# Performance work log

Hardware: AMD Instinct MI355X
Metric: run time of the kernel (lower is better)

The kernel has to match this reference:

```python
import jax, jax.numpy as jnp
import numpy as np
from jax import lax

V, D, H, HD, L, E, HID, TOPK, B, T = 32000, 1024, 16, 64, 2, 4, 2048, 2, 1, 1024
EPS = 1e-8


def setup_inputs() -> dict:
    key = jax.random.key(0)
    ks = jax.random.split(key, 10)
    s = 0.02
    so = 0.02 / np.sqrt(2 * L)  # o_proj / down_proj init std
    return dict(
        idx=jax.random.randint(ks[0], (B, T), 0, V),
        tok_emb=jax.random.normal(ks[1], (V, D), jnp.float32) * s,
        attn_norm_w=jnp.ones((L, D), jnp.float32),
        q_w=jax.random.normal(ks[2], (L, D, D), jnp.float32) * s,
        q_b=jnp.zeros((L, D), jnp.float32),
        kv_w=jax.random.normal(ks[3], (L, D, 2 * D), jnp.float32) * s,
        kv_b=jnp.zeros((L, 2 * D), jnp.float32),
        o_w=jax.random.normal(ks[4], (L, D, D), jnp.float32) * so,
        o_b=jnp.zeros((L, D), jnp.float32),
        ffn_norm_w=jnp.ones((L, D), jnp.float32),
        router_w=jax.random.normal(ks[5], (L, D, E), jnp.float32) * s,
        gate_w=jax.random.normal(ks[6], (L, E, D, HID), jnp.float32) * s,
        up_w=jax.random.normal(ks[7], (L, E, D, HID), jnp.float32) * s,
        down_w=jax.random.normal(ks[8], (L, E, HID, D), jnp.float32) * so,
        lnf_w=jnp.ones((D,), jnp.float32),
    )


def _rms(x, w):
    return x / jnp.sqrt(jnp.mean(x * x, axis=-1, keepdims=True) + EPS) * w


def reference(idx, tok_emb, attn_norm_w, q_w, q_b, kv_w, kv_b, o_w, o_b,
              ffn_norm_w, router_w, gate_w, up_w, down_w, lnf_w):
    x = tok_emb[idx]  # [B,T,D]

    # ALiBi bias and causal mask (built once; block_size == T here)
    slopes = jnp.arange(1, H + 1, dtype=jnp.float32) / H          # [H]
    pos = jnp.arange(T, dtype=jnp.float32)
    alibi = slopes[:, None, None] * (pos[None, None, :] - pos[None, :, None])  # [H,T,T]
    causal = jnp.arange(T)[None, :] > jnp.arange(T)[:, None]      # True above diagonal

    for l in range(L):
        # --- causal self-attention with ALiBi ---
        h = _rms(x, attn_norm_w[l])
        q = (h @ q_w[l] + q_b[l]).reshape(B, T, H, HD)
        kv = (h @ kv_w[l] + kv_b[l]).reshape(B, T, 2, H, HD)
        k, v = kv[:, :, 0], kv[:, :, 1]
        att = jnp.einsum('bqhd,bkhd->bhqk', q, k) * (1.0 / np.sqrt(HD))
        att = att + alibi[None]
        att = jnp.where(causal, -jnp.inf, att)
        a = jax.nn.softmax(att, axis=-1)
        y = jnp.einsum('bhqk,bkhd->bqhd', a, v).reshape(B, T, D)
        x = x + y @ o_w[l] + o_b[l]

        # --- MoE FFN (top-k routing, SwiGLU experts, depth-scaled down_proj) ---
        hm = _rms(x, ffn_norm_w[l]).reshape(B * T, D)             # [N,D]
        rlog = hm @ router_w[l]                                   # [N,E]
        vals, sel = lax.top_k(rlog, TOPK)                         # [N,K]
        w = jax.nn.softmax(vals.astype(jnp.float32), axis=-1).astype(hm.dtype)
        # dense per-expert compute, combined sparsely via routing weights
        g = jax.nn.silu(jnp.einsum('nd,edh->enh', hm, gate_w[l])) \
            * jnp.einsum('nd,edh->enh', hm, up_w[l])              # [E,N,HID]
        out_e = jnp.einsum('enh,ehd->end', g, down_w[l]) * (1.0 / np.sqrt(l + 1))
        combine = jnp.sum(jax.nn.one_hot(sel, E, dtype=hm.dtype) * w[..., None], axis=1)  # [N,E]
        moe = jnp.einsum('ne,end->nd', combine, out_e).reshape(B, T, D)
        x = x + moe

    logits = _rms(x, lnf_w) @ tok_emb.T  # tied head weight
    return logits
```

## Files before the change

### kernel.cpp

```cpp
#include <hip/hip_runtime.h>
#include <cmath>

typedef __attribute__((ext_vector_type(8))) _Float16 f16x8;
typedef __attribute__((ext_vector_type(8))) unsigned short u16x8;
typedef __attribute__((ext_vector_type(4))) float f32x4;

#define DEV static __device__ __forceinline__

constexpr int Dm   = 1024;
constexpr int HIDm = 2048;
constexpr int NT   = 1024;
constexpr int NV   = 32000;
constexpr float EPSf  = 1e-8f;
constexpr float LOSC  = 4096.0f;
constexpr float ILOSC = 1.0f / 4096.0f;

DEV unsigned short h2u(_Float16 h){ union{_Float16 h; unsigned short u;} v; v.h=h; return v.u; }

DEV f32x4 MF(f16x8 a, f16x8 b, f32x4 c){ return __builtin_amdgcn_mfma_f32_16x16x32_f16(a,b,c,0,0,0); }

typedef __attribute__((address_space(1))) void GV;
typedef __attribute__((address_space(3))) void LV;
DEV void gll16(const void* g, void* l){
  __builtin_amdgcn_global_load_lds((GV*)(__UINTPTR_TYPE__)g, (LV*)l, 16, 0, 0);
}

template<int SPLIT>
DEV void st_sp(unsigned short* __restrict__ hi, unsigned short* __restrict__ lo, size_t o, float v){
  _Float16 hh = (_Float16)v;
  hi[o] = h2u(hh);
  if constexpr (SPLIT==3) lo[o] = h2u((_Float16)((v - (float)hh)*LOSC));
}

__global__ __launch_bounds__(256) void k_gather(
    const int* __restrict__ idx, const float* __restrict__ emb, float* __restrict__ x)
{
  const int t = blockIdx.x;
  const int d = threadIdx.x*4;
  *(float4*)&x[(size_t)t*Dm + d] = *(const float4*)&emb[(size_t)idx[t]*Dm + d];
}

template<int SPLIT>
__global__ __launch_bounds__(256) void k_rms(
    const float* __restrict__ x, const float* __restrict__ w,
    unsigned short* __restrict__ ohi, unsigned short* __restrict__ olo)
{
  const int t = blockIdx.x, tid = threadIdx.x;
  const float* row = x + (size_t)t*Dm;
  float s = 0.f;
  #pragma unroll
  for (int i=0;i<4;++i){ const float v = row[tid + i*256]; s += v*v; }
  #pragma unroll
  for (int d=1; d<64; d<<=1) s += __shfl_xor(s, d);
  __shared__ float red[4];
  if ((tid&63)==0) red[tid>>6] = s;
  __syncthreads();
  const float tot = red[0]+red[1]+red[2]+red[3];
  const float rstd = rsqrtf(tot*(1.0f/Dm) + EPSf);
  #pragma unroll
  for (int i=0;i<4;++i){
    const int c = tid + i*256;
    st_sp<SPLIT>(ohi, olo, (size_t)t*Dm + c, row[c]*rstd*w[c]);
  }
}

__global__ __launch_bounds__(64) void k_router(
    const float* __restrict__ x, const float* __restrict__ nw,
    const float* __restrict__ rw, float* __restrict__ cmb)
{
  const int t = blockIdx.x, lane = threadIdx.x;
  const float* row = x + (size_t)t*Dm;
  float ss = 0.f;
  for (int i=lane; i<Dm; i+=64) ss += row[i]*row[i];
  #pragma unroll
  for (int d=1; d<64; d<<=1) ss += __shfl_xor(ss, d);
  const float rstd = rsqrtf(ss*(1.0f/Dm) + EPSf);
  float lg0=0,lg1=0,lg2=0,lg3=0;
  for (int i=lane; i<Dm; i+=64){
    const float hm = row[i]*rstd*nw[i];
    lg0 += hm*rw[i*4+0]; lg1 += hm*rw[i*4+1];
    lg2 += hm*rw[i*4+2]; lg3 += hm*rw[i*4+3];
  }
  #pragma unroll
  for (int d=1; d<64; d<<=1){
    lg0 += __shfl_xor(lg0,d); lg1 += __shfl_xor(lg1,d);
    lg2 += __shfl_xor(lg2,d); lg3 += __shfl_xor(lg3,d);
  }
  if (lane==0){
    float lg[4] = {lg0,lg1,lg2,lg3};
    int s0 = 0;
    for (int e=1;e<4;++e) if (lg[e] > lg[s0]) s0 = e;
    int s1 = -1;
    for (int e=0;e<4;++e){ if (e==s0) continue; if (s1<0 || lg[e] > lg[s1]) s1 = e; }
    const float eb2 = expf(lg[s1] - lg[s0]);
    const float inv = 1.0f/(1.0f + eb2);
    float o[4] = {0.f,0.f,0.f,0.f};
    o[s0] = inv; o[s1] = eb2*inv;
    cmb[t*4+0]=o[0]; cmb[t*4+1]=o[1]; cmb[t*4+2]=o[2]; cmb[t*4+3]=o[3];
  }
}

__global__ __launch_bounds__(256) void k_scan(
    const float* __restrict__ cmb, int* __restrict__ tl,
    float* __restrict__ cwl, int* __restrict__ cnt)
{
  const int e = threadIdx.x>>6, lane = threadIdx.x&63;
  int base = 0;
  for (int t0=0; t0<NT; t0+=64){
    const float w = cmb[(size_t)(t0+lane)*4 + e];
    const unsigned long long m = __ballot(w > 0.f);
    const int pre = __popcll(m & ((1ull<<lane)-1ull));
    if (w > 0.f){ tl[e*NT + base + pre] = t0+lane; cwl[e*NT + base + pre] = w; }
    base += __popcll(m);
  }
  if (lane==0) cnt[e] = base;
}

template<int SPLIT>
__global__ __launch_bounds__(256) void k_wconv(
    const float* __restrict__ W, unsigned short* __restrict__ Whi,
    unsigned short* __restrict__ Wlo, int K, int N)
{
  __shared__ float tile[64][65];
  const int t = threadIdx.x;
  const int n0 = blockIdx.x*64, k0 = blockIdx.y*64;
  const size_t eb = (size_t)blockIdx.z * (size_t)K * N;
  const int r = t>>2;
  #pragma unroll
  for (int i=0;i<4;++i){
    const int c = (t&3)*16 + i*4;
    *(float4*)&tile[r][c] = *(const float4*)&W[eb + (size_t)(k0+r)*N + n0 + c];
  }
  __syncthreads();
  const int n = t>>2;
  #pragma unroll
  for (int i=0;i<2;++i){
    const int kc = (t&3)*8 + i*32;
    u16x8 hi, lo;
    #pragma unroll
    for (int j=0;j<8;++j){
      const float v = tile[kc+j][n];
      const _Float16 hh = (_Float16)v;
      hi[j] = h2u(hh);
      if constexpr (SPLIT==3) lo[j] = h2u((_Float16)((v-(float)hh)*LOSC));
      else lo[j] = 0;
    }
    *(u16x8*)&Whi[eb + (size_t)(n0+n)*K + k0 + kc] = hi;
    if constexpr (SPLIT==3) *(u16x8*)&Wlo[eb + (size_t)(n0+n)*K + k0 + kc] = lo;
  }
}

template<int SPLIT, int EPI, int ZMODE>
__global__ __launch_bounds__(256) void k_mm(
    const unsigned short* __restrict__ Ahi, const unsigned short* __restrict__ Alo,
    const unsigned short* __restrict__ Bhi, const unsigned short* __restrict__ Blo,
    const float* __restrict__ bias, const float* __restrict__ bias2,
    unsigned short* __restrict__ Ohi, unsigned short* __restrict__ Olo,
    unsigned short* __restrict__ O2hi, unsigned short* __restrict__ O2lo,
    unsigned short* __restrict__ O3hi, unsigned short* __restrict__ O3lo,
    float* __restrict__ part, int lda, int ldb, int K)
{
  constexpr int PL = (SPLIT==3)?2:1;
  __shared__ __align__(16) unsigned short As[PL][128][32];
  __shared__ __align__(16) unsigned short Bs[PL][128][32];
  const int tid=threadIdx.x, wv=tid>>6, lane=tid&63, fr=lane&15, fg=lane>>4;
  const int n0=blockIdx.x*128, r0=blockIdx.y*128, zz=blockIdx.z;
  const int wr=(wv>>1)*64, wc=(wv&1)*64;
  const int sr=lane>>2, sk=(lane&3)*8;

  const f32x4 z4={0.f,0.f,0.f,0.f};
  f32x4 accM[4][4], accC[4][4];
  #pragma unroll
  for (int i=0;i<4;++i)
    #pragma unroll
    for (int j=0;j<4;++j){ accM[i][j]=z4; accC[i][j]=z4; }

  for (int kt=0; kt<K; kt+=32){
    #pragma unroll
    for (int i=0;i<2;++i){
      const int rr = wv*32 + i*16 + sr;
      size_t ao, bo;
      if constexpr (ZMODE==2){
        ao = (size_t)(r0+rr)*lda + zz*K + kt + sk;
        bo = (size_t)(n0+rr)*ldb + zz*K + kt + sk;
      } else {
        ao = (size_t)(r0+rr)*lda + kt + sk;
        bo = (size_t)(n0+rr)*ldb + kt + sk;
      }
      gll16(&Ahi[ao], &As[0][wv*32+i*16][0]);
      if constexpr (SPLIT==3) gll16(&Alo[ao], &As[1][wv*32+i*16][0]);
      gll16(&Bhi[bo], &Bs[0][wv*32+i*16][0]);
      if constexpr (SPLIT==3) gll16(&Blo[bo], &Bs[1][wv*32+i*16][0]);
    }
    __syncthreads();
    f16x8 a[4][PL], b[4][PL];
    #pragma unroll
    for (int rt=0;rt<4;++rt)
      #pragma unroll
      for (int p=0;p<PL;++p) a[rt][p] = *(const f16x8*)&As[p][wr+rt*16+fr][fg*8];
    #pragma unroll
    for (int ct=0;ct<4;++ct)
      #pragma unroll
      for (int p=0;p<PL;++p) b[ct][p] = *(const f16x8*)&Bs[p][wc+ct*16+fr][fg*8];
    #pragma unroll
    for (int rt=0;rt<4;++rt)
      #pragma unroll
      for (int ct=0;ct<4;++ct){
        accM[rt][ct] = MF(a[rt][0], b[ct][0], accM[rt][ct]);
        if constexpr (SPLIT==3){
          accC[rt][ct] = MF(a[rt][0], b[ct][1], accC[rt][ct]);
          accC[rt][ct] = MF(a[rt][1], b[ct][0], accC[rt][ct]);
        }
      }
    __syncthreads();
  }

  #pragma unroll
  for (int rt=0;rt<4;++rt)
    #pragma unroll
    for (int ct=0;ct<4;++ct)
      #pragma unroll
      for (int j=0;j<4;++j){
        const int row = r0 + wr + rt*16 + fg*4 + j;
        const int col = n0 + wc + ct*16 + fr;
        float v = accM[rt][ct][j];
        if constexpr (SPLIT==3) v += accC[rt][ct][j]*ILOSC;
        if constexpr (EPI==3){
          if (col < Dm){
            v += bias[col];
            st_sp<SPLIT>(Ohi, Olo, (size_t)row*Dm + col, v);
          } else if (col < 2*Dm){
            v += bias2[col-Dm];
            st_sp<SPLIT>(O2hi, O2lo, (size_t)row*Dm + (col-Dm), v);
          } else {
            v += bias2[col-Dm];
            st_sp<SPLIT>(O3hi, O3lo, (size_t)(col-2*Dm)*NT + row, v);
          }
        } else {
          part[((size_t)zz*NT + row)*Dm + col] = v;
        }
      }
}

template<int SPLIT>
__global__ __launch_bounds__(256) void k_down(
    const unsigned short* __restrict__ Ahi, const unsigned short* __restrict__ Alo,
    const unsigned short* __restrict__ Bhi, const unsigned short* __restrict__ Blo,
    const int* __restrict__ tl, const int* __restrict__ cnt,
    float* __restrict__ part)
{
  constexpr int PL = (SPLIT==3)?2:1;
  const int e = blockIdx.z, r0 = blockIdx.y*128, n0 = blockIdx.x*128;
  const int cn = cnt[e];
  if (r0 >= cn) return;
  __shared__ __align__(16) unsigned short As[PL][128][32];
  __shared__ __align__(16) unsigned short Bs[PL][128][32];
  __shared__ int tl_s[128];
  const int tid=threadIdx.x, wv=tid>>6, lane=tid&63, fr=lane&15, fg=lane>>4;
  const int wr=(wv>>1)*64, wc=(wv&1)*64;
  const int sr=lane>>2, sk=(lane&3)*8;
  if (tid < 128) tl_s[tid] = (r0+tid < cn) ? tl[e*NT + r0 + tid] : -1;

  const f32x4 z4={0.f,0.f,0.f,0.f};
  f32x4 accM[4][4], accC[4][4];
  #pragma unroll
  for (int i=0;i<4;++i)
    #pragma unroll
    for (int j=0;j<4;++j){ accM[i][j]=z4; accC[i][j]=z4; }

  for (int kt=0; kt<HIDm; kt+=32){
    #pragma unroll
    for (int i=0;i<2;++i){
      const int rr = wv*32 + i*16 + sr;
      const size_t ao = (size_t)((e<<10) + r0 + rr)*HIDm + kt + sk;
      const size_t bo = (size_t)e*((size_t)Dm*HIDm) + (size_t)(n0+rr)*HIDm + kt + sk;
      gll16(&Ahi[ao], &As[0][wv*32+i*16][0]);
      if constexpr (SPLIT==3) gll16(&Alo[ao], &As[1][wv*32+i*16][0]);
      gll16(&Bhi[bo], &Bs[0][wv*32+i*16][0]);
      if constexpr (SPLIT==3) gll16(&Blo[bo], &Bs[1][wv*32+i*16][0]);
    }
    __syncthreads();
    f16x8 a[4][PL], b[4][PL];
    #pragma unroll
    for (int rt=0;rt<4;++rt)
      #pragma unroll
      for (int p=0;p<PL;++p) a[rt][p] = *(const f16x8*)&As[p][wr+rt*16+fr][fg*8];
    #pragma unroll
    for (int ct=0;ct<4;++ct)
      #pragma unroll
      for (int p=0;p<PL;++p) b[ct][p] = *(const f16x8*)&Bs[p][wc+ct*16+fr][fg*8];
    #pragma unroll
    for (int rt=0;rt<4;++rt)
      #pragma unroll
      for (int ct=0;ct<4;++ct){
        accM[rt][ct] = MF(a[rt][0], b[ct][0], accM[rt][ct]);
        if constexpr (SPLIT==3){
          accC[rt][ct] = MF(a[rt][0], b[ct][1], accC[rt][ct]);
          accC[rt][ct] = MF(a[rt][1], b[ct][0], accC[rt][ct]);
        }
      }
    __syncthreads();
  }

  #pragma unroll
  for (int rt=0;rt<4;++rt)
    #pragma unroll
    for (int ct=0;ct<4;++ct)
      #pragma unroll
      for (int j=0;j<4;++j){
        const int i = wr + rt*16 + fg*4 + j;
        const int col = n0 + wc + ct*16 + fr;
        float v = accM[rt][ct][j];
        if constexpr (SPLIT==3) v += accC[rt][ct][j]*ILOSC;
        const int tok = tl_s[i];
        if (tok >= 0) part[((size_t)e*NT + tok)*Dm + col] = v;
      }
}

template<int SK, bool BIAS>
__global__ __launch_bounds__(256) void k_comb(
    const float* __restrict__ part, const float* __restrict__ bias, float* __restrict__ x)
{
  const int row = blockIdx.x;
  const int c = threadIdx.x*4;
  float4 s = *(float4*)&x[(size_t)row*Dm + c];
  #pragma unroll
  for (int z=0; z<SK; ++z){
    const float4 p = *(const float4*)&part[((size_t)z*NT + row)*Dm + c];
    s.x+=p.x; s.y+=p.y; s.z+=p.z; s.w+=p.w;
  }
  if constexpr (BIAS){
    const float4 b = *(const float4*)&bias[c];
    s.x+=b.x; s.y+=b.y; s.z+=b.z; s.w+=b.w;
  }
  *(float4*)&x[(size_t)row*Dm + c] = s;
}

__global__ __launch_bounds__(256) void k_comb_moe(
    const float* __restrict__ part, const float* __restrict__ cmb, float* __restrict__ x)
{
  const int row = blockIdx.x;
  const int c = threadIdx.x*4;
  float4 s = *(float4*)&x[(size_t)row*Dm + c];
  #pragma unroll
  for (int e=0; e<4; ++e){
    if (cmb[(size_t)row*4 + e] > 0.f){
      const float4 p = *(const float4*)&part[((size_t)e*NT + row)*Dm + c];
      s.x+=p.x; s.y+=p.y; s.z+=p.z; s.w+=p.w;
    }
  }
  *(float4*)&x[(size_t)row*Dm + c] = s;
}

template<int SPLIT>
__global__ __launch_bounds__(512) void k_guf(
    const unsigned short* __restrict__ Ahi, const unsigned short* __restrict__ Alo,
    const unsigned short* __restrict__ Ghi, const unsigned short* __restrict__ Glo,
    const unsigned short* __restrict__ Uhi, const unsigned short* __restrict__ Ulo,
    const int* __restrict__ tl, const float* __restrict__ cwl, const int* __restrict__ cnt,
    unsigned short* __restrict__ Hhi, unsigned short* __restrict__ Hlo, float scale)
{
  constexpr int PL=(SPLIT==3)?2:1;
  const int e = blockIdx.z, r0 = blockIdx.y*128, n0 = blockIdx.x*64;
  const int cn = cnt[e];
  if (r0 >= cn) return;
  __shared__ __align__(16) unsigned short As[PL][128][32];
  __shared__ __align__(16) unsigned short Gs[PL][64][32];
  __shared__ __align__(16) unsigned short Us[PL][64][32];
  __shared__ float cw_s[128];
  const int tid=threadIdx.x, wv=tid>>6, lane=tid&63, fr=lane&15, fg=lane>>4;
  const int wr=(wv>>1)*32, wc=(wv&1)*32;
  const int sr=lane>>2, sk=(lane&3)*8;
  const size_t ebW = (size_t)e * ((size_t)HIDm*Dm);
  if (tid < 128) cw_s[tid] = (r0+tid < cn) ? cwl[e*NT + r0 + tid]*scale : 0.f;

  const int lrA = r0 + wv*16 + sr;
  const int tokA = tl[e*NT + (lrA < cn ? lrA : cn-1)];
  const size_t abase = (size_t)tokA*Dm + sk;
  const int rrB = (wv&3)*16 + sr;
  const size_t bbase = ebW + (size_t)(n0+rrB)*Dm + sk;

  const f32x4 z4={0.f,0.f,0.f,0.f};
  f32x4 aGM[2][2],aGC[2][2],aUM[2][2],aUC[2][2];
  #pragma unroll
  for (int i=0;i<2;++i)
    #pragma unroll
    for (int j=0;j<2;++j){ aGM[i][j]=z4; aGC[i][j]=z4; aUM[i][j]=z4; aUC[i][j]=z4; }

  for (int kt=0; kt<Dm; kt+=32){
    gll16(&Ahi[abase + kt], &As[0][wv*16][0]);
    if constexpr (SPLIT==3) gll16(&Alo[abase + kt], &As[1][wv*16][0]);
    if (wv < 4){
      gll16(&Ghi[bbase + kt], &Gs[0][(wv&3)*16][0]);
      if constexpr (SPLIT==3) gll16(&Glo[bbase + kt], &Gs[1][(wv&3)*16][0]);
    } else {
      gll16(&Uhi[bbase + kt], &Us[0][(wv&3)*16][0]);
      if constexpr (SPLIT==3) gll16(&Ulo[bbase + kt], &Us[1][(wv&3)*16][0]);
    }
    __syncthreads();
    f16x8 a[2][PL], bg[2][PL], bu[2][PL];
    #pragma unroll
    for (int rt=0;rt<2;++rt)
      #pragma unroll
      for (int p=0;p<PL;++p) a[rt][p] = *(const f16x8*)&As[p][wr+rt*16+fr][fg*8];
    #pragma unroll
    for (int ct=0;ct<2;++ct)
      #pragma unroll
      for (int p=0;p<PL;++p){
        bg[ct][p] = *(const f16x8*)&Gs[p][wc+ct*16+fr][fg*8];
        bu[ct][p] = *(const f16x8*)&Us[p][wc+ct*16+fr][fg*8];
      }
    #pragma unroll
    for (int rt=0;rt<2;++rt)
      #pragma unroll
      for (int ct=0;ct<2;++ct){
        aGM[rt][ct] = MF(a[rt][0], bg[ct][0], aGM[rt][ct]);
        aUM[rt][ct] = MF(a[rt][0], bu[ct][0], aUM[rt][ct]);
        if constexpr (SPLIT==3){
          aGC[rt][ct] = MF(a[rt][0], bg[ct][1], aGC[rt][ct]);
          aGC[rt][ct] = MF(a[rt][1], bg[ct][0], aGC[rt][ct]);
          aUC[rt][ct] = MF(a[rt][0], bu[ct][1], aUC[rt][ct]);
          aUC[rt][ct] = MF(a[rt][1], bu[ct][0], aUC[rt][ct]);
        }
      }
    __syncthreads();
  }
  #pragma unroll
  for (int rt=0;rt<2;++rt)
    #pragma unroll
    for (int ct=0;ct<2;++ct)
      #pragma unroll
      for (int j=0;j<4;++j){
        const int i = wr + rt*16 + fg*4 + j;
        const int row = r0 + i;
        const int col = n0 + wc + ct*16 + fr;
        float g = aGM[rt][ct][j], u = aUM[rt][ct][j];
        if constexpr (SPLIT==3){ g += aGC[rt][ct][j]*ILOSC; u += aUC[rt][ct][j]*ILOSC; }
        const float cw = cw_s[i];
        const float h = (g/(1.0f + expf(-g))) * u * cw;
        st_sp<SPLIT>(Hhi, Hlo, (size_t)((e<<10) + row)*HIDm + col, h);
      }
}

__global__ __launch_bounds__(512) void k_lg(
    const unsigned short* __restrict__ Ahi, const float* __restrict__ emb,
    float* __restrict__ out)
{
  __shared__ __align__(16) unsigned short As[256][32];
  __shared__ __align__(16) unsigned short Bs[256][32];
  const int tid=threadIdx.x, wv=tid>>6, lane=tid&63, fr=lane&15, fg=lane>>4;
  const int bid = blockIdx.x;
  const int n0 = (bid>>2)*256, r0 = (bid&3)*256;
  const int wrow=(wv>>2)*128, wcol=(wv&3)*64;
  const int sr=lane>>2, sk=(lane&3)*8;
  const f32x4 z4={0.f,0.f,0.f,0.f};
  f32x4 acc[8][4];
  #pragma unroll
  for (int i=0;i<8;++i)
    #pragma unroll
    for (int j=0;j<4;++j) acc[i][j]=z4;

  for (int kt=0; kt<Dm; kt+=32){
    #pragma unroll
    for (int i=0;i<2;++i){
      const int rr = wv*32 + i*16 + sr;
      gll16(&Ahi[(size_t)(r0+rr)*Dm + kt + sk], &As[wv*32+i*16][0]);
    }
    #pragma unroll
    for (int i=0;i<2;++i){
      const int br = i*128 + (tid>>2);
      const int bc = (tid&3)*8;
      const float* s = &emb[(size_t)(n0+br)*Dm + kt + bc];
      const float4 v0 = *(const float4*)s;
      const float4 v1 = *(const float4*)(s+4);
      u16x8 hh;
      hh[0]=h2u((_Float16)v0.x); hh[1]=h2u((_Float16)v0.y);
      hh[2]=h2u((_Float16)v0.z); hh[3]=h2u((_Float16)v0.w);
      hh[4]=h2u((_Float16)v1.x); hh[5]=h2u((_Float16)v1.y);
      hh[6]=h2u((_Float16)v1.z); hh[7]=h2u((_Float16)v1.w);
      *(u16x8*)&Bs[br][bc] = hh;
    }
    __syncthreads();
    f16x8 a[8], b[4];
    #pragma unroll
    for (int rt=0;rt<8;++rt) a[rt] = *(const f16x8*)&As[wrow+rt*16+fr][fg*8];
    #pragma unroll
    for (int ct=0;ct<4;++ct) b[ct] = *(const f16x8*)&Bs[wcol+ct*16+fr][fg*8];
    #pragma unroll
    for (int rt=0;rt<8;++rt)
      #pragma unroll
      for (int ct=0;ct<4;++ct) acc[rt][ct] = MF(a[rt], b[ct], acc[rt][ct]);
    __syncthreads();
  }
  #pragma unroll
  for (int rt=0;rt<8;++rt)
    #pragma unroll
    for (int ct=0;ct<4;++ct)
      #pragma unroll
      for (int j=0;j<4;++j)
        out[(size_t)(r0+wrow+rt*16+fg*4+j)*NV + n0+wcol+ct*16+fr] = acc[rt][ct][j];
}

template<int SPLIT>
__global__ __launch_bounds__(256) void k_attn(
    const unsigned short* __restrict__ qhi, const unsigned short* __restrict__ qlo,
    const unsigned short* __restrict__ khi, const unsigned short* __restrict__ klo,
    const unsigned short* __restrict__ vthi, const unsigned short* __restrict__ vtlo,
    unsigned short* __restrict__ yhi, unsigned short* __restrict__ ylo)
{
  constexpr int PL = (SPLIT==3) ? 2 : 1;
  const int qt = blockIdx.x, hd = blockIdx.y;
  const int tid = threadIdx.x, wv = tid>>6, lane = tid&63;
  const int fr = lane&15, fg = lane>>4;
  const int rbase = qt*64 + wv*16;
  const float slope = (float)(hd+1) * (1.0f/16.0f);

  __shared__ __align__(16) unsigned short Ps[4][PL][16][32];

  f16x8 aq[2][PL];
  #pragma unroll
  for (int c=0;c<2;++c){
    const size_t off = (size_t)(rbase+fr)*Dm + hd*64 + c*32 + fg*8;
    aq[c][0] = *(const f16x8*)&qhi[off];
    if constexpr (SPLIT==3) aq[c][1] = *(const f16x8*)&qlo[off];
  }

  const f32x4 z4 = {0.f,0.f,0.f,0.f};
  f32x4 yM[4], yC[4];
  #pragma unroll
  for (int ct=0;ct<4;++ct){ yM[ct]=z4; yC[ct]=z4; }
  float m[4], lsum[4];
  #pragma unroll
  for (int j=0;j<4;++j){ m[j] = -INFINITY; lsum[j] = 0.f; }

  const int nkt = qt*2 + 2;
  for (int kt=0; kt<nkt; ++kt){
    f32x4 sM[2], sC[2];
    sM[0]=z4; sM[1]=z4; sC[0]=z4; sC[1]=z4;
    #pragma unroll
    for (int kh=0; kh<2; ++kh){
      #pragma unroll
      for (int c=0;c<2;++c){
        const size_t off = (size_t)(kt*32 + kh*16 + fr)*Dm + hd*64 + c*32 + fg*8;
        const f16x8 b0 = *(const f16x8*)&khi[off];
        sM[kh] = MF(aq[c][0], b0, sM[kh]);
        if constexpr (SPLIT==3){
          const f16x8 b1 = *(const f16x8*)&klo[off];
          sC[kh] = MF(aq[c][0], b1, sC[kh]);
          sC[kh] = MF(aq[c][1], b0, sC[kh]);
        }
      }
    }
    float sv[2][4], mx[4];
    #pragma unroll
    for (int j=0;j<4;++j) mx[j] = -INFINITY;
    #pragma unroll
    for (int kh=0; kh<2; ++kh)
      #pragma unroll
      for (int j=0;j<4;++j){
        const int kcol = kt*32 + kh*16 + fr;
        const int row  = rbase + fg*4 + j;
        float s = sM[kh][j];
        if constexpr (SPLIT==3) s += sC[kh][j]*ILOSC;
        s = s*0.125f + slope*(float)(kcol - row);
        sv[kh][j] = (kcol > row) ? -INFINITY : s;
        mx[j] = fmaxf(mx[j], sv[kh][j]);
      }
    #pragma unroll
    for (int d=1; d<16; d<<=1)
      #pragma unroll
      for (int j=0;j<4;++j) mx[j] = fmaxf(mx[j], __shfl_xor(mx[j], d));
    float resc[4];
    #pragma unroll
    for (int j=0;j<4;++j){
      const float mn = fmaxf(m[j], mx[j]);
      resc[j] = expf(m[j] - mn);
      m[j] = mn;
    }
    float p[2][4], psum[4];
    #pragma unroll
    for (int j=0;j<4;++j) psum[j] = 0.f;
    #pragma unroll
    for (int kh=0;kh<2;++kh)
      #pragma unroll
      for (int j=0;j<4;++j){
        const float pv = (sv[kh][j] == -INFINITY) ? 0.f : expf(sv[kh][j] - m[j]);
        p[kh][j] = pv; psum[j] += pv;
      }
    #pragma unroll
    for (int d=1; d<16; d<<=1)
      #pragma unroll
      for (int j=0;j<4;++j) psum[j] += __shfl_xor(psum[j], d);
    #pragma unroll
    for (int j=0;j<4;++j) lsum[j] = lsum[j]*resc[j] + psum[j];
    #pragma unroll
    for (int ct=0;ct<4;++ct)
      #pragma unroll
      for (int j=0;j<4;++j){ yM[ct][j]*=resc[j]; yC[ct][j]*=resc[j]; }
    #pragma unroll
    for (int kh=0;kh<2;++kh)
      #pragma unroll
      for (int j=0;j<4;++j){
        const float pv = p[kh][j];
        _Float16 ph = (_Float16)pv;
        Ps[wv][0][fg*4+j][kh*16+fr] = h2u(ph);
        if constexpr (SPLIT==3)
          Ps[wv][1][fg*4+j][kh*16+fr] = h2u((_Float16)((pv-(float)ph)*LOSC));
      }
    asm volatile("s_waitcnt lgkmcnt(0)" ::: "memory");
    f16x8 pa[PL];
    pa[0] = *(const f16x8*)&Ps[wv][0][fr][fg*8];
    if constexpr (SPLIT==3) pa[1] = *(const f16x8*)&Ps[wv][1][fr][fg*8];
    #pragma unroll
    for (int ct=0;ct<4;++ct){
      const size_t off = (size_t)(hd*64 + ct*16 + fr)*NT + kt*32 + fg*8;
      const f16x8 v0 = *(const f16x8*)&vthi[off];
      yM[ct] = MF(pa[0], v0, yM[ct]);
      if constexpr (SPLIT==3){
        const f16x8 v1 = *(const f16x8*)&vtlo[off];
        yC[ct] = MF(pa[0], v1, yC[ct]);
        yC[ct] = MF(pa[1], v0, yC[ct]);
      }
    }
    asm volatile("s_waitcnt lgkmcnt(0)" ::: "memory");
  }
  #pragma unroll
  for (int ct=0;ct<4;++ct)
    #pragma unroll
    for (int j=0;j<4;++j){
      float v = yM[ct][j];
      if constexpr (SPLIT==3) v += yC[ct][j]*ILOSC;
      v /= lsum[j];
      const size_t off = (size_t)(rbase + fg*4 + j)*Dm + hd*64 + ct*16 + fr;
      st_sp<SPLIT>(yhi, ylo, off, v);
    }
}

struct Ptrs {
  float* x; float* cmb; float* part; float* cwl; int* tl; int* cnt;
  unsigned short *hhi,*hlo,*qhi,*qlo,*khi,*klo,*vthi,*vtlo,*yhi,*ylo,*Hhi,*Hlo;
  unsigned short *Wqkvh,*Wqkvl,*WOh,*WOl,*WGh,*WGl,*WUh,*WUl,*WDh,*WDl;
};

template<int S>
static void run_layer(const Ptrs& P, int l,
    const float* anw, const float* qw, const float* qb, const float* kvw, const float* kvb,
    const float* ow, const float* ob, const float* fnw, const float* rw,
    const float* gw, const float* uw, const float* dw, float scale, hipStream_t stream)
{
  unsigned short* nul = nullptr;
  k_rms<S><<<dim3(NT), dim3(256), 0, stream>>>(P.x, anw + l*Dm, P.hhi, P.hlo);
  k_wconv<S><<<dim3(16,16,1), dim3(256), 0, stream>>>(qw + (size_t)l*Dm*Dm, P.Wqkvh, P.Wqkvl, Dm, Dm);
  k_wconv<S><<<dim3(32,16,1), dim3(256), 0, stream>>>(kvw + (size_t)l*Dm*2*Dm,
      P.Wqkvh + (size_t)Dm*Dm, P.Wqkvl + (size_t)Dm*Dm, Dm, 2*Dm);
  k_wconv<S><<<dim3(16,16,1), dim3(256), 0, stream>>>(ow + (size_t)l*Dm*Dm, P.WOh, P.WOl, Dm, Dm);
  k_mm<S,3,0><<<dim3(24,8), dim3(256), 0, stream>>>(P.hhi, P.hlo, P.Wqkvh, P.Wqkvl,
      qb + l*Dm, kvb + l*2*Dm, P.qhi, P.qlo, P.khi, P.klo, P.vthi, P.vtlo,
      nullptr, Dm, Dm, Dm);
  k_attn<S><<<dim3(16,16), dim3(256), 0, stream>>>(P.qhi,P.qlo,P.khi,P.klo,P.vthi,P.vtlo,P.yhi,P.ylo);
  k_mm<S,4,2><<<dim3(8,8,4), dim3(256), 0, stream>>>(P.yhi, P.ylo, P.WOh, P.WOl,
      nullptr, nullptr, nul, nul, nul, nul, nul, nul, P.part, Dm, Dm, 256);
  k_comb<4,true><<<dim3(NT), dim3(256), 0, stream>>>(P.part, ob + l*Dm, P.x);
  k_router<<<dim3(NT), dim3(64), 0, stream>>>(P.x, fnw + l*Dm, rw + (size_t)l*Dm*4, P.cmb);
  k_scan<<<dim3(1), dim3(256), 0, stream>>>(P.cmb, P.tl, P.cwl, P.cnt);
  k_rms<S><<<dim3(NT), dim3(256), 0, stream>>>(P.x, fnw + l*Dm, P.hhi, P.hlo);
  k_wconv<S><<<dim3(32,16,4), dim3(256), 0, stream>>>(gw + (size_t)l*4*Dm*HIDm, P.WGh, P.WGl, Dm, HIDm);
  k_wconv<S><<<dim3(32,16,4), dim3(256), 0, stream>>>(uw + (size_t)l*4*Dm*HIDm, P.WUh, P.WUl, Dm, HIDm);
  k_guf<S><<<dim3(32,8,4), dim3(512), 0, stream>>>(P.hhi, P.hlo, P.WGh, P.WGl, P.WUh, P.WUl,
      P.tl, P.cwl, P.cnt, P.Hhi, P.Hlo, scale);
  k_wconv<S><<<dim3(16,32,4), dim3(256), 0, stream>>>(dw + (size_t)l*4*HIDm*Dm, P.WDh, P.WDl, HIDm, Dm);
  k_down<S><<<dim3(8,8,4), dim3(256), 0, stream>>>(P.Hhi, P.Hlo, P.WDh, P.WDl,
      P.tl, P.cnt, P.part);
  k_comb_moe<<<dim3(NT), dim3(256), 0, stream>>>(P.part, P.cmb, P.x);
}

extern "C" void kernel_launch(void* const* d_in, const int* in_sizes, int n_in,
                              void* d_out, int out_size, void* d_ws, size_t ws_size,
                              hipStream_t stream)
{
  (void)in_sizes; (void)n_in; (void)out_size; (void)ws_size;
  const int*   idx = (const int*)d_in[0];
  const float* emb = (const float*)d_in[1];
  const float* anw = (const float*)d_in[2];
  const float* qw  = (const float*)d_in[3];
  const float* qb  = (const float*)d_in[4];
  const float* kvw = (const float*)d_in[5];
  const float* kvb = (const float*)d_in[6];
  const float* ow  = (const float*)d_in[7];
  const float* ob  = (const float*)d_in[8];
  const float* fnw = (const float*)d_in[9];
  const float* rw  = (const float*)d_in[10];
  const float* gw  = (const float*)d_in[11];
  const float* uw  = (const float*)d_in[12];
  const float* dw  = (const float*)d_in[13];
  const float* lnf = (const float*)d_in[14];

  constexpr size_t MB = (size_t)1<<20;
  constexpr size_t KB = (size_t)1<<10;
  char* sc = (char*)d_out;
  Ptrs P;
  P.x     = (float*)sc;
  P.hhi   = (unsigned short*)(sc + 4*MB);
  P.hlo   = (unsigned short*)(sc + 6*MB);
  P.qhi   = (unsigned short*)(sc + 8*MB);
  P.qlo   = (unsigned short*)(sc + 10*MB);
  P.khi   = (unsigned short*)(sc + 12*MB);
  P.klo   = (unsigned short*)(sc + 14*MB);
  P.vthi  = (unsigned short*)(sc + 16*MB);
  P.vtlo  = (unsigned short*)(sc + 18*MB);
  P.yhi   = (unsigned short*)(sc + 20*MB);
  P.ylo   = (unsigned short*)(sc + 22*MB);
  P.cmb   = (float*)(sc + 24*MB);
  P.tl    = (int*)(sc + 24*MB + 64*KB);
  P.cwl   = (float*)(sc + 24*MB + 128*KB);
  P.cnt   = (int*)(sc + 24*MB + 192*KB);
  P.Hhi   = (unsigned short*)(sc + 25*MB);
  P.Hlo   = (unsigned short*)(sc + 41*MB);
  P.Wqkvh = (unsigned short*)(sc + 57*MB);
  P.Wqkvl = (unsigned short*)(sc + 63*MB);
  P.WOh   = (unsigned short*)(sc + 69*MB);
  P.WOl   = (unsigned short*)(sc + 71*MB);
  P.WGh   = (unsigned short*)(sc + 57*MB);
  P.WGl   = (unsigned short*)(sc + 73*MB);
  P.WUh   = (unsigned short*)(sc + 89*MB);
  P.WUl   = (unsigned short*)(sc + 105*MB);
  P.WDh   = (unsigned short*)(sc + 57*MB);
  P.WDl   = (unsigned short*)(sc + 73*MB);
  P.part  = (float*)(sc + 89*MB);
  unsigned short* xhat = (unsigned short*)d_ws;
  float* out = (float*)d_out;

  k_gather<<<dim3(NT), dim3(256), 0, stream>>>(idx, emb, P.x);

  run_layer<3>(P, 0, anw, qw, qb, kvw, kvb, ow, ob, fnw, rw, gw, uw, dw, 1.0f, stream);
  run_layer<1>(P, 1, anw, qw, qb, kvw, kvb, ow, ob, fnw, rw, gw, uw, dw, 0.70710678f, stream);

  k_rms<1><<<dim3(NT), dim3(256), 0, stream>>>(P.x, lnf, xhat, nullptr);
  k_lg<<<dim3(500), dim3(512), 0, stream>>>(xhat, emb, out);
}
```

Baseline: 896.7 us.

## Split-K the QKV and down projections and shrink logits tiles for more blocks

```diff
diff --git a/kernel.cpp b/kernel.cpp
--- a/kernel.cpp
+++ b/kernel.cpp
@@ -150,15 +150,11 @@
   }
 }
 
-template<int SPLIT, int EPI, int ZMODE>
+template<int SPLIT, int ZMODE>
 __global__ __launch_bounds__(256) void k_mm(
     const unsigned short* __restrict__ Ahi, const unsigned short* __restrict__ Alo,
     const unsigned short* __restrict__ Bhi, const unsigned short* __restrict__ Blo,
-    const float* __restrict__ bias, const float* __restrict__ bias2,
-    unsigned short* __restrict__ Ohi, unsigned short* __restrict__ Olo,
-    unsigned short* __restrict__ O2hi, unsigned short* __restrict__ O2lo,
-    unsigned short* __restrict__ O3hi, unsigned short* __restrict__ O3lo,
-    float* __restrict__ part, int lda, int ldb, int K)
+    float* __restrict__ part, int lda, int ldb, int K, int ldo)
 {
   constexpr int PL = (SPLIT==3)?2:1;
   __shared__ __align__(16) unsigned short As[PL][128][32];
@@ -225,21 +221,70 @@
         const int col = n0 + wc + ct*16 + fr;
         float v = accM[rt][ct][j];
         if constexpr (SPLIT==3) v += accC[rt][ct][j]*ILOSC;
-        if constexpr (EPI==3){
-          if (col < Dm){
-            v += bias[col];
-            st_sp<SPLIT>(Ohi, Olo, (size_t)row*Dm + col, v);
-          } else if (col < 2*Dm){
-            v += bias2[col-Dm];
-            st_sp<SPLIT>(O2hi, O2lo, (size_t)row*Dm + (col-Dm), v);
-          } else {
-            v += bias2[col-Dm];
-            st_sp<SPLIT>(O3hi, O3lo, (size_t)(col-2*Dm)*NT + row, v);
-          }
-        } else {
-          part[((size_t)zz*NT + row)*Dm + col] = v;
-        }
-      }
+        part[((size_t)zz*NT + row)*ldo + col] = v;
+      }
+}
+
+template<int SPLIT>
+__global__ __launch_bounds__(256) void k_comb_qk(
+    const float* __restrict__ part, const float* __restrict__ qb, const float* __restrict__ kvb,
+    unsigned short* __restrict__ qhi, unsigned short* __restrict__ qlo,
+    unsigned short* __restrict__ khi, unsigned short* __restrict__ klo)
+{
+  const int t = blockIdx.x;
+  #pragma unroll
+  for (int i=0;i<2;++i){
+    const int col = threadIdx.x*4 + i*1024;
+    const float4 p0 = *(const float4*)&part[(size_t)t*3072 + col];
+    const float4 p1 = *(const float4*)&part[((size_t)NT + t)*3072 + col];
+    float v[4] = {p0.x+p1.x, p0.y+p1.y, p0.z+p1.z, p0.w+p1.w};
+    #pragma unroll
+    for (int j=0;j<4;++j){
+      const int c = col + j;
+      if (c < Dm) st_sp<SPLIT>(qhi, qlo, (size_t)t*Dm + c, v[j] + qb[c]);
+      else        st_sp<SPLIT>(khi, klo, (size_t)t*Dm + (c-Dm), v[j] + kvb[c-Dm]);
+    }
+  }
+}
+
+template<int SPLIT>
+__global__ __launch_bounds__(256) void k_combvT(
+    const float* __restrict__ part, const float* __restrict__ kvb,
+    unsigned short* __restrict__ vthi, unsigned short* __restrict__ vtlo)
+{
+  __shared__ float tile[64][65];
+  const int d0 = blockIdx.x*64, t0 = blockIdx.y*64;
+  const int tid = threadIdx.x;
+  {
+    const int tl_ = tid>>2, dc = (tid&3)*16;
+    #pragma unroll
+    for (int i=0;i<4;++i){
+      const int d = dc + i*4;
+      const float4 p0 = *(const float4*)&part[(size_t)(t0+tl_)*3072 + 2048 + d0 + d];
+      const float4 p1 = *(const float4*)&part[((size_t)NT + t0+tl_)*3072 + 2048 + d0 + d];
+      tile[tl_][d+0] = p0.x+p1.x + kvb[1024+d0+d+0];
+      tile[tl_][d+1] = p0.y+p1.y + kvb[1024+d0+d+1];
+      tile[tl_][d+2] = p0.z+p1.z + kvb[1024+d0+d+2];
+      tile[tl_][d+3] = p0.w+p1.w + kvb[1024+d0+d+3];
+    }
+  }
+  __syncthreads();
+  #pragma unroll
+  for (int i=0;i<2;++i){
+    const int u = tid + i*256;
+    const int dl = u>>3, tch = (u&7)*8;
+    u16x8 hi, lo;
+    #pragma unroll
+    for (int j=0;j<8;++j){
+      const float v = tile[tch+j][dl];
+      const _Float16 hh = (_Float16)v;
+      hi[j] = h2u(hh);
+      if constexpr (SPLIT==3) lo[j] = h2u((_Float16)((v-(float)hh)*LOSC));
+      else lo[j] = 0;
+    }
+    *(u16x8*)&vthi[(size_t)(d0+dl)*NT + t0 + tch] = hi;
+    if constexpr (SPLIT==3) *(u16x8*)&vtlo[(size_t)(d0+dl)*NT + t0 + tch] = lo;
+  }
 }
 
 template<int SPLIT>
@@ -250,7 +295,8 @@
     float* __restrict__ part)
 {
   constexpr int PL = (SPLIT==3)?2:1;
-  const int e = blockIdx.z, r0 = blockIdx.y*128, n0 = blockIdx.x*128;
+  const int zz = blockIdx.z, e = zz>>1, ks = zz&1;
+  const int r0 = blockIdx.y*128, n0 = blockIdx.x*128;
   const int cn = cnt[e];
   if (r0 >= cn) return;
   __shared__ __align__(16) unsigned short As[PL][128][32];
@@ -268,7 +314,8 @@
     #pragma unroll
     for (int j=0;j<4;++j){ accM[i][j]=z4; accC[i][j]=z4; }
 
-  for (int kt=0; kt<HIDm; kt+=32){
+  const int kbeg = ks*1024, kend = kbeg + 1024;
+  for (int kt=kbeg; kt<kend; kt+=32){
     #pragma unroll
     for (int i=0;i<2;++i){
       const int rr = wv*32 + i*16 + sr;
@@ -313,7 +360,7 @@
         float v = accM[rt][ct][j];
         if constexpr (SPLIT==3) v += accC[rt][ct][j]*ILOSC;
         const int tok = tl_s[i];
-        if (tok >= 0) part[((size_t)e*NT + tok)*Dm + col] = v;
+        if (tok >= 0) part[((size_t)zz*NT + tok)*Dm + col] = v;
       }
 }
 
@@ -345,8 +392,9 @@
   #pragma unroll
   for (int e=0; e<4; ++e){
     if (cmb[(size_t)row*4 + e] > 0.f){
-      const float4 p = *(const float4*)&part[((size_t)e*NT + row)*Dm + c];
-      s.x+=p.x; s.y+=p.y; s.z+=p.z; s.w+=p.w;
+      const float4 p0 = *(const float4*)&part[((size_t)(e*2+0)*NT + row)*Dm + c];
+      const float4 p1 = *(const float4*)&part[((size_t)(e*2+1)*NT + row)*Dm + c];
+      s.x+=p0.x+p1.x; s.y+=p0.y+p1.y; s.z+=p0.z+p1.z; s.w+=p0.w+p1.w;
     }
   }
   *(float4*)&x[(size_t)row*Dm + c] = s;
@@ -442,21 +490,22 @@
       }
 }
 
-__global__ __launch_bounds__(512) void k_lg(
+__global__ __launch_bounds__(256) void k_lg(
     const unsigned short* __restrict__ Ahi, const float* __restrict__ emb,
     float* __restrict__ out)
 {
-  __shared__ __align__(16) unsigned short As[256][32];
-  __shared__ __align__(16) unsigned short Bs[256][32];
+  __shared__ __align__(16) unsigned short As[128][32];
+  __shared__ __align__(16) unsigned short Bs[128][32];
   const int tid=threadIdx.x, wv=tid>>6, lane=tid&63, fr=lane&15, fg=lane>>4;
   const int bid = blockIdx.x;
-  const int n0 = (bid>>2)*256, r0 = (bid&3)*256;
-  const int wrow=(wv>>2)*128, wcol=(wv&3)*64;
+  const int n0 = (bid>>3)*128, r0 = (bid&7)*128;
+  const int wr=(wv>>1)*64, wc=(wv&1)*64;
   const int sr=lane>>2, sk=(lane&3)*8;
+  const int br = tid>>1, bc = (tid&1)*16;
   const f32x4 z4={0.f,0.f,0.f,0.f};
-  f32x4 acc[8][4];
-  #pragma unroll
-  for (int i=0;i<8;++i)
+  f32x4 acc[4][4];
+  #pragma unroll
+  for (int i=0;i<4;++i)
     #pragma unroll
     for (int j=0;j<4;++j) acc[i][j]=z4;
 
@@ -466,39 +515,43 @@
       const int rr = wv*32 + i*16 + sr;
       gll16(&Ahi[(size_t)(r0+rr)*Dm + kt + sk], &As[wv*32+i*16][0]);
     }
-    #pragma unroll
-    for (int i=0;i<2;++i){
-      const int br = i*128 + (tid>>2);
-      const int bc = (tid&3)*8;
+    {
       const float* s = &emb[(size_t)(n0+br)*Dm + kt + bc];
       const float4 v0 = *(const float4*)s;
       const float4 v1 = *(const float4*)(s+4);
-      u16x8 hh;
-      hh[0]=h2u((_Float16)v0.x); hh[1]=h2u((_Float16)v0.y);
-      hh[2]=h2u((_Float16)v0.z); hh[3]=h2u((_Float16)v0.w);
-      hh[4]=h2u((_Float16)v1.x); hh[5]=h2u((_Float16)v1.y);
-      hh[6]=h2u((_Float16)v1.z); hh[7]=h2u((_Float16)v1.w);
-      *(u16x8*)&Bs[br][bc] = hh;
+      const float4 v2 = *(const float4*)(s+8);
+      const float4 v3 = *(const float4*)(s+12);
+      u16x8 h0, h1;
+      h0[0]=h2u((_Float16)v0.x); h0[1]=h2u((_Float16)v0.y);
+      h0[2]=h2u((_Float16)v0.z); h0[3]=h2u((_Float16)v0.w);
+      h0[4]=h2u((_Float16)v1.x); h0[5]=h2u((_Float16)v1.y);
+      h0[6]=h2u((_Float16)v1.z); h0[7]=h2u((_Float16)v1.w);
+      h1[0]=h2u((_Float16)v2.x); h1[1]=h2u((_Float16)v2.y);
+      h1[2]=h2u((_Float16)v2.z); h1[3]=h2u((_Float16)v2.w);
+      h1[4]=h2u((_Float16)v3.x); h1[5]=h2u((_Float16)v3.y);
+      h1[6]=h2u((_Float16)v3.z); h1[7]=h2u((_Float16)v3.w);
+      *(u16x8*)&Bs[br][bc]   = h0;
+      *(u16x8*)&Bs[br][bc+8] = h1;
     }
     __syncthreads();
-    f16x8 a[8], b[4];
-    #pragma unroll
-    for (int rt=0;rt<8;++rt) a[rt] = *(const f16x8*)&As[wrow+rt*16+fr][fg*8];
-    #pragma unroll
-    for (int ct=0;ct<4;++ct) b[ct] = *(const f16x8*)&Bs[wcol+ct*16+fr][fg*8];
-    #pragma unroll
-    for (int rt=0;rt<8;++rt)
+    f16x8 a[4], b[4];
+    #pragma unroll
+    for (int rt=0;rt<4;++rt) a[rt] = *(const f16x8*)&As[wr+rt*16+fr][fg*8];
+    #pragma unroll
+    for (int ct=0;ct<4;++ct) b[ct] = *(const f16x8*)&Bs[wc+ct*16+fr][fg*8];
+    #pragma unroll
+    for (int rt=0;rt<4;++rt)
       #pragma unroll
       for (int ct=0;ct<4;++ct) acc[rt][ct] = MF(a[rt], b[ct], acc[rt][ct]);
     __syncthreads();
   }
   #pragma unroll
-  for (int rt=0;rt<8;++rt)
+  for (int rt=0;rt<4;++rt)
     #pragma unroll
     for (int ct=0;ct<4;++ct)
       #pragma unroll
       for (int j=0;j<4;++j)
-        out[(size_t)(r0+wrow+rt*16+fg*4+j)*NV + n0+wcol+ct*16+fr] = acc[rt][ct][j];
+        out[(size_t)(r0+wr+rt*16+fg*4+j)*NV + n0+wc+ct*16+fr] = acc[rt][ct][j];
 }
 
 template<int SPLIT>
@@ -648,18 +701,19 @@
     const float* ow, const float* ob, const float* fnw, const float* rw,
     const float* gw, const float* uw, const float* dw, float scale, hipStream_t stream)
 {
-  unsigned short* nul = nullptr;
   k_rms<S><<<dim3(NT), dim3(256), 0, stream>>>(P.x, anw + l*Dm, P.hhi, P.hlo);
   k_wconv<S><<<dim3(16,16,1), dim3(256), 0, stream>>>(qw + (size_t)l*Dm*Dm, P.Wqkvh, P.Wqkvl, Dm, Dm);
   k_wconv<S><<<dim3(32,16,1), dim3(256), 0, stream>>>(kvw + (size_t)l*Dm*2*Dm,
       P.Wqkvh + (size_t)Dm*Dm, P.Wqkvl + (size_t)Dm*Dm, Dm, 2*Dm);
   k_wconv<S><<<dim3(16,16,1), dim3(256), 0, stream>>>(ow + (size_t)l*Dm*Dm, P.WOh, P.WOl, Dm, Dm);
-  k_mm<S,3,0><<<dim3(24,8), dim3(256), 0, stream>>>(P.hhi, P.hlo, P.Wqkvh, P.Wqkvl,
-      qb + l*Dm, kvb + l*2*Dm, P.qhi, P.qlo, P.khi, P.klo, P.vthi, P.vtlo,
-      nullptr, Dm, Dm, Dm);
+  k_mm<S,2><<<dim3(24,8,2), dim3(256), 0, stream>>>(P.hhi, P.hlo, P.Wqkvh, P.Wqkvl,
+      P.part, Dm, Dm, 512, 3072);
+  k_comb_qk<S><<<dim3(NT), dim3(256), 0, stream>>>(P.part, qb + l*Dm, kvb + l*2*Dm,
+      P.qhi, P.qlo, P.khi, P.klo);
+  k_combvT<S><<<dim3(16,16), dim3(256), 0, stream>>>(P.part, kvb + l*2*Dm, P.vthi, P.vtlo);
   k_attn<S><<<dim3(16,16), dim3(256), 0, stream>>>(P.qhi,P.qlo,P.khi,P.klo,P.vthi,P.vtlo,P.yhi,P.ylo);
-  k_mm<S,4,2><<<dim3(8,8,4), dim3(256), 0, stream>>>(P.yhi, P.ylo, P.WOh, P.WOl,
-      nullptr, nullptr, nul, nul, nul, nul, nul, nul, P.part, Dm, Dm, 256);
+  k_mm<S,2><<<dim3(8,8,4), dim3(256), 0, stream>>>(P.yhi, P.ylo, P.WOh, P.WOl,
+      P.part, Dm, Dm, 256, Dm);
   k_comb<4,true><<<dim3(NT), dim3(256), 0, stream>>>(P.part, ob + l*Dm, P.x);
   k_router<<<dim3(NT), dim3(64), 0, stream>>>(P.x, fnw + l*Dm, rw + (size_t)l*Dm*4, P.cmb);
   k_scan<<<dim3(1), dim3(256), 0, stream>>>(P.cmb, P.tl, P.cwl, P.cnt);
@@ -669,7 +723,7 @@
   k_guf<S><<<dim3(32,8,4), dim3(512), 0, stream>>>(P.hhi, P.hlo, P.WGh, P.WGl, P.WUh, P.WUl,
       P.tl, P.cwl, P.cnt, P.Hhi, P.Hlo, scale);
   k_wconv<S><<<dim3(16,32,4), dim3(256), 0, stream>>>(dw + (size_t)l*4*HIDm*Dm, P.WDh, P.WDl, HIDm, Dm);
-  k_down<S><<<dim3(8,8,4), dim3(256), 0, stream>>>(P.Hhi, P.Hlo, P.WDh, P.WDl,
+  k_down<S><<<dim3(8,8,8), dim3(256), 0, stream>>>(P.Hhi, P.Hlo, P.WDh, P.WDl,
       P.tl, P.cnt, P.part);
   k_comb_moe<<<dim3(NT), dim3(256), 0, stream>>>(P.part, P.cmb, P.x);
 }
@@ -736,5 +790,5 @@
   run_layer<1>(P, 1, anw, qw, qb, kvw, kvb, ow, ob, fnw, rw, gw, uw, dw, 0.70710678f, stream);
 
   k_rms<1><<<dim3(NT), dim3(256), 0, stream>>>(P.x, lnf, xhat, nullptr);
-  k_lg<<<dim3(500), dim3(512), 0, stream>>>(xhat, emb, out);
-}
+  k_lg<<<dim3(2000), dim3(256), 0, stream>>>(xhat, emb, out);
+}
```

After: 867.9 us. -3.2%, faster.
